# Kernel tuning notes

Hardware: AMD Instinct MI355X
Metric: run time of the kernel (lower is better)

Reference implementation:

```python
import jax, jax.numpy as jnp
import numpy as np

EPS = 1e-8
N, D, B, L = 50000, 128, 64, 512
P0, P1, NEG_MS = 200000, 50000, 4


def setup_inputs() -> dict:
    key = jax.random.key(0)
    ks = jax.random.split(key, 14)
    return {
        "embeddings": jax.random.normal(ks[0], (N, D), jnp.float32) * 0.1,
        "W_rep": jax.random.normal(ks[1], (D, 2), jnp.float32) * 0.01,
        "W_q": jax.random.normal(ks[2], (D, D), jnp.float32) * 0.01,
        "W_k": jax.random.normal(ks[3], (D, D), jnp.float32) * 0.01,
        "W_v": jax.random.normal(ks[4], (D, D), jnp.float32) * 0.01,
        "Head_agg": jax.random.normal(ks[5], (D, D), jnp.float32) * 0.01,
        "user_init": jax.random.normal(ks[6], (1, D), jnp.float32) * 0.01,
        "sd_e0": jnp.ones((), jnp.float32),
        "sd_e1": jnp.ones((), jnp.float32),
        "sd_seq": jnp.ones((), jnp.float32),
        "pos_e0": jax.random.randint(ks[7], (P0, 2), 0, N, jnp.int32),
        "neg_e0": jax.random.randint(ks[8], (P0, 2), 0, N, jnp.int32),
        "pos_e1": jax.random.randint(ks[9], (P1, 2), 0, N, jnp.int32),
        "neg_e1": jax.random.randint(ks[10], (P1 * NEG_MS, 2), 0, N, jnp.int32),
        "q_seqs": jax.random.randint(ks[11], (B, L), 0, N, jnp.int32),
        "c_seqs": jax.random.randint(ks[12], (B, L), 0, 2, jnp.int32),
        "neg_ms": NEG_MS,
    }


def _logsig(x):
    return jnp.log(jax.nn.sigmoid(x) + EPS)


def _task_term(loss, p_t, sd):
    return loss / (sd ** 2 + EPS) + p_t * jnp.log(sd + EPS)


def _forward(embeddings, W_rep, W_q, W_k, W_v, Head_agg, user_init,
             sd_e0, sd_e1, sd_seq,
             pos_e0, neg_e0, pos_e1, neg_e1, q_seqs, c_seqs, neg_ms):
    d = embeddings.shape[1]
    scale = 1.0 / jnp.sqrt(jnp.asarray(d, jnp.float32))

    # ---- edge type e0: complete ----
    ph0 = embeddings[pos_e0[:, 0]]
    pt0 = embeddings[pos_e0[:, 1]]
    nh0 = embeddings[neg_e0[:, 0]]
    nt0 = embeddings[neg_e0[:, 1]]
    pos_score0 = jnp.sum(ph0 * pt0, axis=1)
    neg_score0 = jnp.sum(nh0 * nt0, axis=1)
    loss0 = -(_logsig(pos_score0).sum() + _logsig(-neg_score0).sum())
    p_t0 = pos_e0.shape[0] + neg_e0.shape[0]
    tf_loss = _task_term(loss0, p_t0, sd_e0)

    # ---- edge type e1: incomplete (pairwise ranking) ----
    ph1 = jnp.tile(embeddings[pos_e1[:, 0]], (neg_ms, 1))   # [P1*neg_ms, D]
    pt1 = jnp.tile(embeddings[pos_e1[:, 1]], (neg_ms, 1))
    nh1 = embeddings[neg_e1[:, 0]]
    nt1 = embeddings[neg_e1[:, 1]]
    pos_score1 = jnp.sum(ph1 * pt1, axis=1)
    neg_score_h = jnp.sum(nh1 * pt1, axis=1)
    neg_score_t = jnp.sum(ph1 * nt1, axis=1)
    loss1 = -(_logsig(pos_score1 - neg_score_h).sum() +
              _logsig(pos_score1 - neg_score_t).sum())
    p_t1 = neg_e1.shape[0] * 2
    tf_loss = tf_loss + _task_term(loss1, p_t1, sd_e1)

    # ---- per-user single-head causal attention (batched via vmap) ----
    seq_len = q_seqs.shape[1]
    idx = jnp.arange(seq_len)
    # mask[i, j] = 0 if j >= i else -inf (softmax over i => attend to i <= j)
    mask = jnp.where(idx[:, None] <= idx[None, :], 0.0, -jnp.inf)

    def one_user(q_s, c_s):
        I_q = embeddings[q_s].T                 # [D, L]
        I = W_rep[:, c_s] + I_q                 # [D, L]
        q = W_q @ I                             # [D, L]
        k = W_k @ I
        v = W_v @ I
        score = (k.T @ q) * scale               # [L, L], score[i, j] = k_i . q_j
        att = jax.nn.softmax(score + mask, axis=0)
        b = v @ att                             # [D, L]
        o = Head_agg @ b                        # [D, L]
        u_state = jnp.concatenate([user_init, o.T], axis=0)  # [L+1, D]
        return u_state[:-1, :], I_q.T           # ([L, D], [L, D])

    u_state_b, q_state_b = jax.vmap(one_user)(q_seqs, c_seqs)  # [B, L, D]
    u_flat = u_state_b.reshape(-1, d)
    q_flat = q_state_b.reshape(-1, d)
    c_flat = c_seqs.reshape(-1).astype(jnp.float32)
    pred = jax.nn.sigmoid(jnp.sum(u_flat * q_flat, axis=1))
    seq_loss = -(c_flat * jnp.log(pred + EPS) +
                 (1.0 - c_flat) * jnp.log(1.0 - pred + EPS)).sum()
    p_t_seq = seq_len  # original uses length of the LAST user's sequence
    tf_loss = tf_loss + _task_term(seq_loss, p_t_seq, sd_seq)
    return tf_loss


def reference(embeddings, W_rep, W_q, W_k, W_v, Head_agg, user_init,
              sd_e0, sd_e1, sd_seq,
              pos_e0, neg_e0, pos_e1, neg_e1, q_seqs, c_seqs, neg_ms):
    return _forward(embeddings, W_rep, W_q, W_k, W_v, Head_agg, user_init,
                    sd_e0, sd_e1, sd_seq,
                    pos_e0, neg_e0, pos_e1, neg_e1, q_seqs, c_seqs, neg_ms)
```

## Files before the change

### kernel.cpp

```cpp
#include <hip/hip_runtime.h>
#include <hip/hip_bf16.h>

#define EPSF 1e-8f
#define NN 50000
#define DD 128
#define BB 64
#define LL 512
#define PP0 200000
#define PP1 50000
#define SCALE 0.08838834764831845f

typedef float f4v __attribute__((ext_vector_type(4)));
typedef short s8v __attribute__((ext_vector_type(8)));
typedef short s4v __attribute__((ext_vector_type(4)));

__device__ __forceinline__ float logsigf(float x) {
    float s = 1.f / (1.f + __expf(-x));
    return __logf(s + EPSF);
}

__device__ __forceinline__ float red64(float v) {
    #pragma unroll
    for (int m = 32; m >= 1; m >>= 1) v += __shfl_xor(v, m, 64);
    return v;
}
__device__ __forceinline__ float red16(float v) {
    #pragma unroll
    for (int m = 8; m >= 1; m >>= 1) v += __shfl_xor(v, m, 64);
    return v;
}
__device__ __forceinline__ float red8(float v) {
    #pragma unroll
    for (int m = 4; m >= 1; m >>= 1) v += __shfl_xor(v, m, 64);
    return v;
}

__device__ __forceinline__ void block_atomic_sum(float local, float* dst) {
    local = red64(local);
    __shared__ float w4[4];
    if ((threadIdx.x & 63) == 0) w4[threadIdx.x >> 6] = local;
    __syncthreads();
    if (threadIdx.x == 0) atomicAdd(dst, w4[0] + w4[1] + w4[2] + w4[3]);
}

__device__ __forceinline__ unsigned short f2bf(float f) {
    unsigned u = __float_as_uint(f);
    unsigned r = (u + 0x7fffu + ((u >> 16) & 1u)) >> 16;
    return (unsigned short)r;
}
__device__ __forceinline__ float bf2f(unsigned short u) {
    return __uint_as_float(((unsigned)u) << 16);
}

__device__ __forceinline__ float dot8bf(s8v a, s8v b) {
    float s = 0.f;
    #pragma unroll
    for (int j = 0; j < 8; j++)
        s += bf2f((unsigned short)a[j]) * bf2f((unsigned short)b[j]);
    return s;
}

__global__ __launch_bounds__(256) void cvt_emb_kernel(
    const float* __restrict__ emb, unsigned short* __restrict__ emb16)
{
    int stride = gridDim.x * 256 * 8;
    for (int i = (blockIdx.x * 256 + threadIdx.x) * 8; i < NN * DD; i += stride) {
        float4 a = *(const float4*)&emb[i];
        float4 b = *(const float4*)&emb[i + 4];
        s8v o;
        o[0] = (short)f2bf(a.x); o[1] = (short)f2bf(a.y);
        o[2] = (short)f2bf(a.z); o[3] = (short)f2bf(a.w);
        o[4] = (short)f2bf(b.x); o[5] = (short)f2bf(b.y);
        o[6] = (short)f2bf(b.z); o[7] = (short)f2bf(b.w);
        *(s8v*)&emb16[i] = o;
    }
}

__global__ __launch_bounds__(256) void cvt_w_kernel(
    const float* __restrict__ Wq, const float* __restrict__ Wk,
    const float* __restrict__ Wv, const float* __restrict__ Hd,
    unsigned short* __restrict__ W16)
{
    int idx = (blockIdx.x * 256 + threadIdx.x) * 8;
    int which = idx >> 14, off = idx & 16383;
    const float* src = (which == 0) ? Wq : (which == 1) ? Wk : (which == 2) ? Wv : Hd;
    float4 a = *(const float4*)&src[off];
    float4 b = *(const float4*)&src[off + 4];
    s8v o;
    o[0] = (short)f2bf(a.x); o[1] = (short)f2bf(a.y);
    o[2] = (short)f2bf(a.z); o[3] = (short)f2bf(a.w);
    o[4] = (short)f2bf(b.x); o[5] = (short)f2bf(b.y);
    o[6] = (short)f2bf(b.z); o[7] = (short)f2bf(b.w);
    *(s8v*)&W16[idx] = o;
}

#define E0B 1024
#define E1B 640
__global__ __launch_bounds__(256) void edges_kernel(
    const unsigned short* __restrict__ emb16, const int* __restrict__ pos,
    const int* __restrict__ neg, const int* __restrict__ pos1,
    const int* __restrict__ neg1, float* __restrict__ acc)
{
    if (blockIdx.x < E0B) {
        int sub = threadIdx.x & 7;
        int g0 = (blockIdx.x * 256 + threadIdx.x) >> 3;
        const int ng = E0B * 32;
        float local = 0.f;
        for (int grp = g0; grp < 2 * PP0; grp += ng) {
            bool isneg = grp >= PP0;
            const int* e = isneg ? (neg + 2 * (grp - PP0)) : (pos + 2 * grp);
            int h = e[0], t = e[1];
            const unsigned short* hr = emb16 + (size_t)h * DD + 16 * sub;
            const unsigned short* tr = emb16 + (size_t)t * DD + 16 * sub;
            s8v a0 = *(const s8v*)&hr[0];
            s8v a1 = *(const s8v*)&hr[8];
            s8v b0 = *(const s8v*)&tr[0];
            s8v b1 = *(const s8v*)&tr[8];
            float d = red8(dot8bf(a0, b0) + dot8bf(a1, b1));
            if (sub == 0) local += logsigf(isneg ? -d : d);
        }
        block_atomic_sum(local, acc);
    } else {
        int sub = threadIdx.x & 15;
        int g0 = ((blockIdx.x - E0B) * 256 + threadIdx.x) >> 4;
        const int ng = E1B * 16;
        float local = 0.f;
        for (int i = g0; i < PP1; i += ng) {
            int ph = pos1[2 * i], pt = pos1[2 * i + 1];
            s8v vph = *(const s8v*)&emb16[(size_t)ph * DD + 8 * sub];
            s8v vpt = *(const s8v*)&emb16[(size_t)pt * DD + 8 * sub];
            float ps = red16(dot8bf(vph, vpt));
            #pragma unroll
            for (int mloop = 0; mloop < 4; mloop++) {
                int g = mloop * PP1 + i;
                int nh = neg1[2 * g], nt = neg1[2 * g + 1];
                s8v vnh = *(const s8v*)&emb16[(size_t)nh * DD + 8 * sub];
                s8v vnt = *(const s8v*)&emb16[(size_t)nt * DD + 8 * sub];
                float sh = red16(dot8bf(vnh, vpt));
                float st = red16(dot8bf(vph, vnt));
                if (sub == 0) local += logsigf(ps - sh) + logsigf(ps - st);
            }
        }
        block_atomic_sum(local, acc + 1);
    }
}

__global__ __launch_bounds__(256) void proj_kernel(
    const unsigned short* __restrict__ emb16, const float* __restrict__ Wrep,
    const unsigned short* __restrict__ W16, const int* __restrict__ qseq,
    const int* __restrict__ cseq, unsigned short* __restrict__ QT16,
    unsigned short* __restrict__ KT16, unsigned short* __restrict__ VT16T)
{
    int b = blockIdx.y;
    int t0 = blockIdx.x * 64;
    __shared__ unsigned short Itok[64 * 136];
    __shared__ unsigned short Wl[128 * 136];
    __shared__ int qs[64];
    __shared__ int cs[64];
    int tid = threadIdx.x;
    if (tid < 64) {
        qs[tid] = qseq[b * LL + t0 + tid];
        cs[tid] = cseq[b * LL + t0 + tid];
    }
    __syncthreads();
    {
        int t = tid >> 2, d0 = (tid & 3) * 32;
        const unsigned short* er = emb16 + (size_t)qs[t] * DD + d0;
        int c = cs[t];
        #pragma unroll
        for (int e = 0; e < 32; e += 8) {
            s8v raw = *(const s8v*)&er[e];
            s8v o;
            #pragma unroll
            for (int j = 0; j < 8; j++) {
                float f = bf2f((unsigned short)raw[j]) + Wrep[(d0 + e + j) * 2 + c];
                o[j] = (short)f2bf(f);
            }
            *(s8v*)&Itok[t * 136 + d0 + e] = o;
        }
    }
    int w = tid >> 6, lane = tid & 63, n = lane & 15, quad = lane >> 4;

    for (int w3 = 0; w3 < 3; w3++) {
        __syncthreads();
        {
            const unsigned short* src = W16 + w3 * DD * DD + (tid >> 1) * DD + (tid & 1) * 64;
            unsigned short* dst = &Wl[(tid >> 1) * 136 + (tid & 1) * 64];
            #pragma unroll
            for (int e = 0; e < 64; e += 8)
                *(s8v*)&dst[e] = *(const s8v*)&src[e];
        }
        __syncthreads();
        f4v a2[2][4];
        #pragma unroll
        for (int mt = 0; mt < 2; mt++)
            #pragma unroll
            for (int nt = 0; nt < 4; nt++) a2[mt][nt] = (f4v){0.f, 0.f, 0.f, 0.f};
        #pragma unroll
        for (int c = 0; c < 4; c++) {
            s8v af0 = *(const s8v*)&Wl[(w * 32 + n) * 136 + c * 32 + quad * 8];
            s8v af1 = *(const s8v*)&Wl[(w * 32 + 16 + n) * 136 + c * 32 + quad * 8];
            #pragma unroll
            for (int nt = 0; nt < 4; nt++) {
                s8v bf = *(const s8v*)&Itok[(nt * 16 + n) * 136 + c * 32 + quad * 8];
                a2[0][nt] = __builtin_amdgcn_mfma_f32_16x16x32_bf16(af0, bf, a2[0][nt], 0, 0, 0);
                a2[1][nt] = __builtin_amdgcn_mfma_f32_16x16x32_bf16(af1, bf, a2[1][nt], 0, 0, 0);
            }
        }
        if (w3 < 2) {
            unsigned short* OUT = (w3 == 0) ? QT16 : KT16;
            #pragma unroll
            for (int mt = 0; mt < 2; mt++)
                #pragma unroll
                for (int nt = 0; nt < 4; nt++) {
                    int t = t0 + nt * 16 + n;
                    int r = w * 32 + mt * 16 + quad * 4;
                    s4v o;
                    #pragma unroll
                    for (int rr = 0; rr < 4; rr++) o[rr] = (short)f2bf(a2[mt][nt][rr]);
                    *(s4v*)&OUT[((size_t)(b * LL) + t) * DD + r] = o;
                }
        } else {
            __syncthreads();
            #pragma unroll
            for (int mt = 0; mt < 2; mt++)
                #pragma unroll
                for (int nt = 0; nt < 4; nt++) {
                    int tl = nt * 16 + n;
                    int r = w * 32 + mt * 16 + quad * 4;
                    #pragma unroll
                    for (int rr = 0; rr < 4; rr++)
                        Wl[(r + rr) * 72 + tl] = f2bf(a2[mt][nt][rr]);
                }
            __syncthreads();
            int row = tid >> 1, half = tid & 1;
            unsigned short* gdst = VT16T + ((size_t)b * DD + row) * LL + t0 + half * 32;
            const unsigned short* lsrc = &Wl[row * 72 + half * 32];
            #pragma unroll
            for (int e = 0; e < 32; e += 8)
                *(s8v*)&gdst[e] = *(const s8v*)&lsrc[e];
        }
    }
}

__global__ __launch_bounds__(256) void attn_mfma_kernel(
    const unsigned short* __restrict__ QT16, const unsigned short* __restrict__ KT16,
    const unsigned short* __restrict__ VT16T, float* __restrict__ BvT)
{
    int id = blockIdx.x;
    int r0 = id & 255;
    int b = r0 & 63;
    int qt = (id >> 8) ? (7 - (r0 >> 6)) : (r0 >> 6);

    __shared__ unsigned short K_lds[64 * 136];
    __shared__ unsigned short Vt_lds[128 * 72];
    __shared__ unsigned short P_lds[64 * 72];

    int tid = threadIdx.x;
    int w = tid >> 6;
    int lane = tid & 63;
    int n = lane & 15;
    int quad = lane >> 4;
    int gj = qt * 64 + w * 16 + n;

    s8v qfrag[4];
    {
        const unsigned short* qrow = QT16 + ((size_t)(b * LL) + gj) * DD;
        #pragma unroll
        for (int c = 0; c < 4; c++)
            qfrag[c] = *(const s8v*)&qrow[c * 32 + quad * 8];
    }

    f4v oacc[8];
    #pragma unroll
    for (int dt = 0; dt < 8; dt++) oacc[dt] = (f4v){0.f, 0.f, 0.f, 0.f};
    float m_run = -INFINITY, l_run = 0.f;

    s8v kreg[4], vreg[4];
    #pragma unroll
    for (int rep = 0; rep < 4; rep++) {
        int idx = rep * 2048 + tid * 8;
        int ki = idx >> 7, kd = idx & 127;
        kreg[rep] = *(const s8v*)&KT16[((size_t)(b * LL) + ki) * DD + kd];
        int vr = idx >> 6, vc = idx & 63;
        vreg[rep] = *(const s8v*)&VT16T[((size_t)b * DD + vr) * LL + vc];
    }

    for (int kt = 0; kt <= qt; ++kt) {
        __syncthreads();
        #pragma unroll
        for (int rep = 0; rep < 4; rep++) {
            int idx = rep * 2048 + tid * 8;
            int ki = idx >> 7, kd = idx & 127;
            *(s8v*)&K_lds[ki * 136 + kd] = kreg[rep];
            int vr = idx >> 6, vc = idx & 63;
            *(s8v*)&Vt_lds[vr * 72 + vc] = vreg[rep];
        }
        __syncthreads();
        if (kt < qt) {
            #pragma unroll
            for (int rep = 0; rep < 4; rep++) {
                int idx = rep * 2048 + tid * 8;
                int ki = idx >> 7, kd = idx & 127;
                kreg[rep] = *(const s8v*)&KT16[((size_t)(b * LL) + (kt + 1) * 64 + ki) * DD + kd];
                int vr = idx >> 6, vc = idx & 63;
                vreg[rep] = *(const s8v*)&VT16T[((size_t)b * DD + vr) * LL + (kt + 1) * 64 + vc];
            }
        }

        f4v sacc[4];
        #pragma unroll
        for (int mt = 0; mt < 4; mt++) sacc[mt] = (f4v){0.f, 0.f, 0.f, 0.f};
        #pragma unroll
        for (int c = 0; c < 4; c++) {
            #pragma unroll
            for (int mt = 0; mt < 4; mt++) {
                s8v af = *(const s8v*)&K_lds[(mt * 16 + n) * 136 + c * 32 + quad * 8];
                sacc[mt] = __builtin_amdgcn_mfma_f32_16x16x32_bf16(af, qfrag[c], sacc[mt], 0, 0, 0);
            }
        }

        bool diag = (kt == qt);
        float mloc = -INFINITY;
        #pragma unroll
        for (int mt = 0; mt < 4; mt++) {
            #pragma unroll
            for (int rr = 0; rr < 4; rr++) {
                float s = sacc[mt][rr] * SCALE;
                if (diag && (kt * 64 + mt * 16 + quad * 4 + rr) > gj) s = -INFINITY;
                sacc[mt][rr] = s;
                mloc = fmaxf(mloc, s);
            }
        }
        mloc = fmaxf(mloc, __shfl_xor(mloc, 16));
        mloc = fmaxf(mloc, __shfl_xor(mloc, 32));
        float mnew = fmaxf(m_run, mloc);
        float alpha = __expf(m_run - mnew);
        m_run = mnew;

        float rsum = 0.f;
        #pragma unroll
        for (int mt = 0; mt < 4; mt++) {
            s4v pp;
            #pragma unroll
            for (int rr = 0; rr < 4; rr++) {
                float p = __expf(sacc[mt][rr] - mnew);
                rsum += p;
                pp[rr] = (short)f2bf(p);
            }
            *(s4v*)&P_lds[(w * 16 + n) * 72 + mt * 16 + quad * 4] = pp;
        }
        rsum += __shfl_xor(rsum, 16);
        rsum += __shfl_xor(rsum, 32);
        l_run = l_run * alpha + rsum;

        #pragma unroll
        for (int rr = 0; rr < 4; rr++) {
            float a_r = __shfl(alpha, quad * 4 + rr);
            #pragma unroll
            for (int dt = 0; dt < 8; dt++) oacc[dt][rr] *= a_r;
        }

        #pragma unroll
        for (int cc = 0; cc < 2; cc++) {
            s8v pf = *(const s8v*)&P_lds[(w * 16 + n) * 72 + cc * 32 + quad * 8];
            #pragma unroll
            for (int dt = 0; dt < 8; dt++) {
                s8v vf = *(const s8v*)&Vt_lds[(dt * 16 + n) * 72 + cc * 32 + quad * 8];
                oacc[dt] = __builtin_amdgcn_mfma_f32_16x16x32_bf16(pf, vf, oacc[dt], 0, 0, 0);
            }
        }
    }

    float linv = 1.f / l_run;
    #pragma unroll
    for (int rr = 0; rr < 4; rr++) {
        float li = __shfl(linv, quad * 4 + rr);
        int t = qt * 64 + w * 16 + quad * 4 + rr;
        float* orow = BvT + ((size_t)(b * LL) + t) * DD;
        #pragma unroll
        for (int dt = 0; dt < 8; dt++)
            orow[dt * 16 + n] = oacc[dt][rr] * li;
    }
}

__global__ __launch_bounds__(256) void head_kernel(
    const unsigned short* __restrict__ H16, const float* __restrict__ BvT,
    const unsigned short* __restrict__ emb16, const float* __restrict__ uinit,
    const int* __restrict__ qseq, const int* __restrict__ cseq,
    float* __restrict__ acc)
{
    int b = blockIdx.y;
    int t0 = blockIdx.x * 64;
    __shared__ unsigned short Btok[64 * 136];
    __shared__ unsigned short Hl[128 * 136];
    __shared__ unsigned short O_lds[64 * 136];
    int tid = threadIdx.x;
    {
        int t = tid >> 2, d0 = (tid & 3) * 32;
        const float* br = BvT + ((size_t)(b * LL) + t0 + t) * DD + d0;
        #pragma unroll
        for (int e = 0; e < 32; e += 8) {
            float4 x = *(const float4*)&br[e];
            float4 y = *(const float4*)&br[e + 4];
            s8v o;
            o[0] = (short)f2bf(x.x); o[1] = (short)f2bf(x.y);
            o[2] = (short)f2bf(x.z); o[3] = (short)f2bf(x.w);
            o[4] = (short)f2bf(y.x); o[5] = (short)f2bf(y.y);
            o[6] = (short)f2bf(y.z); o[7] = (short)f2bf(y.w);
            *(s8v*)&Btok[t * 136 + d0 + e] = o;
        }
    }
    {
        const unsigned short* src = H16 + (tid >> 1) * DD + (tid & 1) * 64;
        unsigned short* dst = &Hl[(tid >> 1) * 136 + (tid & 1) * 64];
        #pragma unroll
        for (int e = 0; e < 64; e += 8)
            *(s8v*)&dst[e] = *(const s8v*)&src[e];
    }
    __syncthreads();

    int w = tid >> 6, lane = tid & 63, n = lane & 15, quad = lane >> 4;
    f4v a2[2][4];
    #pragma unroll
    for (int mt = 0; mt < 2; mt++)
        #pragma unroll
        for (int nt = 0; nt < 4; nt++) a2[mt][nt] = (f4v){0.f, 0.f, 0.f, 0.f};
    #pragma unroll
    for (int c = 0; c < 4; c++) {
        s8v af0 = *(const s8v*)&Hl[(w * 32 + n) * 136 + c * 32 + quad * 8];
        s8v af1 = *(const s8v*)&Hl[(w * 32 + 16 + n) * 136 + c * 32 + quad * 8];
        #pragma unroll
        for (int nt = 0; nt < 4; nt++) {
            s8v bf = *(const s8v*)&Btok[(nt * 16 + n) * 136 + c * 32 + quad * 8];
            a2[0][nt] = __builtin_amdgcn_mfma_f32_16x16x32_bf16(af0, bf, a2[0][nt], 0, 0, 0);
            a2[1][nt] = __builtin_amdgcn_mfma_f32_16x16x32_bf16(af1, bf, a2[1][nt], 0, 0, 0);
        }
    }
    #pragma unroll
    for (int mt = 0; mt < 2; mt++)
        #pragma unroll
        for (int nt = 0; nt < 4; nt++) {
            int tl = nt * 16 + n;
            int r = w * 32 + mt * 16 + quad * 4;
            #pragma unroll
            for (int rr = 0; rr < 4; rr++)
                O_lds[tl * 136 + r + rr] = f2bf(a2[mt][nt][rr]);
        }
    __syncthreads();

    int g = tid >> 4, sub = tid & 15;
    float local = 0.f;
    #pragma unroll
    for (int tt = 0; tt < 4; tt++) {
        int tl = g * 4 + tt;
        int t = t0 + tl + 1;
        if (t < LL) {
            s8v uv = *(const s8v*)&O_lds[tl * 136 + sub * 8];
            int qi = qseq[b * LL + t];
            s8v ev = *(const s8v*)&emb16[(size_t)qi * DD + sub * 8];
            float s = red16(dot8bf(uv, ev));
            if (sub == 0) {
                float c = (float)cseq[b * LL + t];
                float pred = 1.f / (1.f + __expf(-s));
                local += c * __logf(pred + EPSF) + (1.f - c) * __logf(1.f - pred + EPSF);
            }
        }
    }
    if (t0 == 0 && g == 0) {
        int qi = qseq[b * LL];
        s8v ev = *(const s8v*)&emb16[(size_t)qi * DD + sub * 8];
        float4 u0 = *(const float4*)&uinit[sub * 8];
        float4 u1 = *(const float4*)&uinit[sub * 8 + 4];
        float s = u0.x * bf2f((unsigned short)ev[0]) + u0.y * bf2f((unsigned short)ev[1])
                + u0.z * bf2f((unsigned short)ev[2]) + u0.w * bf2f((unsigned short)ev[3])
                + u1.x * bf2f((unsigned short)ev[4]) + u1.y * bf2f((unsigned short)ev[5])
                + u1.z * bf2f((unsigned short)ev[6]) + u1.w * bf2f((unsigned short)ev[7]);
        s = red16(s);
        if (sub == 0) {
            float c = (float)cseq[b * LL];
            float pred = 1.f / (1.f + __expf(-s));
            local += c * __logf(pred + EPSF) + (1.f - c) * __logf(1.f - pred + EPSF);
        }
    }
    block_atomic_sum(local, acc + 2);
}

__global__ void combine_kernel(
    const float* __restrict__ acc, const float* __restrict__ sd0p,
    const float* __restrict__ sd1p, const float* __restrict__ sdqp,
    float* __restrict__ out)
{
    if (threadIdx.x == 0 && blockIdx.x == 0) {
        float l0 = -acc[0], l1 = -acc[1], ls = -acc[2];
        float s0 = *sd0p, s1 = *sd1p, ss = *sdqp;
        float tf = l0 / (s0 * s0 + EPSF) + 400000.f * logf(s0 + EPSF)
                 + l1 / (s1 * s1 + EPSF) + 400000.f * logf(s1 + EPSF)
                 + ls / (ss * ss + EPSF) + 512.f * logf(ss + EPSF);
        out[0] = tf;
    }
}

extern "C" void kernel_launch(void* const* d_in, const int* in_sizes, int n_in,
                              void* d_out, int out_size, void* d_ws, size_t ws_size,
                              hipStream_t stream) {
    const float* emb   = (const float*)d_in[0];
    const float* Wrep  = (const float*)d_in[1];
    const float* Wq    = (const float*)d_in[2];
    const float* Wk    = (const float*)d_in[3];
    const float* Wv    = (const float*)d_in[4];
    const float* Hd    = (const float*)d_in[5];
    const float* uinit = (const float*)d_in[6];
    const float* sd0   = (const float*)d_in[7];
    const float* sd1   = (const float*)d_in[8];
    const float* sdq   = (const float*)d_in[9];
    const int* pe0 = (const int*)d_in[10];
    const int* ne0 = (const int*)d_in[11];
    const int* pe1 = (const int*)d_in[12];
    const int* ne1 = (const int*)d_in[13];
    const int* qs  = (const int*)d_in[14];
    const int* cs  = (const int*)d_in[15];

    const size_t SZ = (size_t)BB * LL * DD;
    char* base = (char*)d_ws;
    float* acc = (float*)base;
    unsigned short* emb16 = (unsigned short*)(base + 256);
    unsigned short* W16   = emb16 + (size_t)NN * DD;
    unsigned short* QT16  = W16 + 4 * DD * DD;
    unsigned short* KT16  = QT16 + SZ;
    unsigned short* VT16T = KT16 + SZ;
    float* BvT = (float*)(VT16T + SZ);

    hipMemsetAsync(acc, 0, 256, stream);

    cvt_emb_kernel<<<1024, 256, 0, stream>>>(emb, emb16);
    cvt_w_kernel<<<32, 256, 0, stream>>>(Wq, Wk, Wv, Hd, W16);

    edges_kernel<<<E0B + E1B, 256, 0, stream>>>(emb16, pe0, ne0, pe1, ne1, acc);

    proj_kernel<<<dim3(8, 64), 256, 0, stream>>>(emb16, Wrep, W16, qs, cs,
                                                 QT16, KT16, VT16T);
    attn_mfma_kernel<<<512, 256, 0, stream>>>(QT16, KT16, VT16T, BvT);
    head_kernel<<<dim3(8, 64), 256, 0, stream>>>(W16 + 3 * DD * DD, BvT,
                                                 emb16, uinit, qs, cs, acc);

    combine_kernel<<<1, 64, 0, stream>>>(acc, sd0, sd1, sdq, (float*)d_out);
}
```

Before: 206.4 us.

## Spread edge-loss blocks across projection, attention and head kernels

Removes the standalone edges kernel and splits its 1664 blocks among the proj, attn and head launches as extra blocks (416+896+352), so the irregular gather-bound edge work runs alongside the compute-bound sequence kernels. Also removes the weight conversion kernel by converting fp32 weights to bf16 while staging them into LDS, and reuses Btok in place of a separate O_lds buffer. This saves launches and fills idle CUs, but adds redundant weight conversion per block and risks load imbalance or lower occupancy in the fused kernels.

```diff
diff --git a/kernel.cpp b/kernel.cpp
--- a/kernel.cpp
+++ b/kernel.cpp
@@ -10,6 +10,12 @@
 #define PP1 50000
 #define SCALE 0.08838834764831845f
 
+#define G0B 1024
+#define G1B 640
+#define EK2 416
+#define EK3 896
+#define EK4 352
+
 typedef float f4v __attribute__((ext_vector_type(4)));
 typedef short s8v __attribute__((ext_vector_type(8)));
 typedef short s4v __attribute__((ext_vector_type(4)));
@@ -58,6 +64,55 @@
     for (int j = 0; j < 8; j++)
         s += bf2f((unsigned short)a[j]) * bf2f((unsigned short)b[j]);
     return s;
+}
+
+__device__ void edge_slice(int eid, const unsigned short* __restrict__ emb16,
+                           const int* __restrict__ pos, const int* __restrict__ neg,
+                           const int* __restrict__ pos1, const int* __restrict__ neg1,
+                           float* __restrict__ acc)
+{
+    if (eid < G0B) {
+        int sub = threadIdx.x & 7;
+        int g0 = eid * 32 + (threadIdx.x >> 3);
+        const int ng = G0B * 32;
+        float local = 0.f;
+        for (int grp = g0; grp < 2 * PP0; grp += ng) {
+            bool isneg = grp >= PP0;
+            const int* e = isneg ? (neg + 2 * (grp - PP0)) : (pos + 2 * grp);
+            int h = e[0], t = e[1];
+            const unsigned short* hr = emb16 + (size_t)h * DD + 16 * sub;
+            const unsigned short* tr = emb16 + (size_t)t * DD + 16 * sub;
+            s8v a0 = *(const s8v*)&hr[0];
+            s8v a1 = *(const s8v*)&hr[8];
+            s8v b0 = *(const s8v*)&tr[0];
+            s8v b1 = *(const s8v*)&tr[8];
+            float d = red8(dot8bf(a0, b0) + dot8bf(a1, b1));
+            if (sub == 0) local += logsigf(isneg ? -d : d);
+        }
+        block_atomic_sum(local, acc);
+    } else {
+        int sub = threadIdx.x & 15;
+        int g0 = (eid - G0B) * 16 + (threadIdx.x >> 4);
+        const int ng = G1B * 16;
+        float local = 0.f;
+        for (int i = g0; i < PP1; i += ng) {
+            int ph = pos1[2 * i], pt = pos1[2 * i + 1];
+            s8v vph = *(const s8v*)&emb16[(size_t)ph * DD + 8 * sub];
+            s8v vpt = *(const s8v*)&emb16[(size_t)pt * DD + 8 * sub];
+            float ps = red16(dot8bf(vph, vpt));
+            #pragma unroll
+            for (int mloop = 0; mloop < 4; mloop++) {
+                int g = mloop * PP1 + i;
+                int nh = neg1[2 * g], nt = neg1[2 * g + 1];
+                s8v vnh = *(const s8v*)&emb16[(size_t)nh * DD + 8 * sub];
+                s8v vnt = *(const s8v*)&emb16[(size_t)nt * DD + 8 * sub];
+                float sh = red16(dot8bf(vnh, vpt));
+                float st = red16(dot8bf(vph, vnt));
+                if (sub == 0) local += logsigf(ps - sh) + logsigf(ps - st);
+            }
+        }
+        block_atomic_sum(local, acc + 1);
+    }
 }
 
 __global__ __launch_bounds__(256) void cvt_emb_kernel(
@@ -76,83 +131,22 @@
     }
 }
 
-__global__ __launch_bounds__(256) void cvt_w_kernel(
+__global__ __launch_bounds__(256) void proj_edges_kernel(
+    const unsigned short* __restrict__ emb16, const float* __restrict__ Wrep,
     const float* __restrict__ Wq, const float* __restrict__ Wk,
-    const float* __restrict__ Wv, const float* __restrict__ Hd,
-    unsigned short* __restrict__ W16)
+    const float* __restrict__ Wv, const int* __restrict__ qseq,
+    const int* __restrict__ cseq, unsigned short* __restrict__ QT16,
+    unsigned short* __restrict__ KT16, unsigned short* __restrict__ VT16T,
+    const int* __restrict__ pos, const int* __restrict__ neg,
+    const int* __restrict__ pos1, const int* __restrict__ neg1,
+    float* __restrict__ acc)
 {
-    int idx = (blockIdx.x * 256 + threadIdx.x) * 8;
-    int which = idx >> 14, off = idx & 16383;
-    const float* src = (which == 0) ? Wq : (which == 1) ? Wk : (which == 2) ? Wv : Hd;
-    float4 a = *(const float4*)&src[off];
-    float4 b = *(const float4*)&src[off + 4];
-    s8v o;
-    o[0] = (short)f2bf(a.x); o[1] = (short)f2bf(a.y);
-    o[2] = (short)f2bf(a.z); o[3] = (short)f2bf(a.w);
-    o[4] = (short)f2bf(b.x); o[5] = (short)f2bf(b.y);
-    o[6] = (short)f2bf(b.z); o[7] = (short)f2bf(b.w);
-    *(s8v*)&W16[idx] = o;
-}
-
-#define E0B 1024
-#define E1B 640
-__global__ __launch_bounds__(256) void edges_kernel(
-    const unsigned short* __restrict__ emb16, const int* __restrict__ pos,
-    const int* __restrict__ neg, const int* __restrict__ pos1,
-    const int* __restrict__ neg1, float* __restrict__ acc)
-{
-    if (blockIdx.x < E0B) {
-        int sub = threadIdx.x & 7;
-        int g0 = (blockIdx.x * 256 + threadIdx.x) >> 3;
-        const int ng = E0B * 32;
-        float local = 0.f;
-        for (int grp = g0; grp < 2 * PP0; grp += ng) {
-            bool isneg = grp >= PP0;
-            const int* e = isneg ? (neg + 2 * (grp - PP0)) : (pos + 2 * grp);
-            int h = e[0], t = e[1];
-            const unsigned short* hr = emb16 + (size_t)h * DD + 16 * sub;
-            const unsigned short* tr = emb16 + (size_t)t * DD + 16 * sub;
-            s8v a0 = *(const s8v*)&hr[0];
-            s8v a1 = *(const s8v*)&hr[8];
-            s8v b0 = *(const s8v*)&tr[0];
-            s8v b1 = *(const s8v*)&tr[8];
-            float d = red8(dot8bf(a0, b0) + dot8bf(a1, b1));
-            if (sub == 0) local += logsigf(isneg ? -d : d);
-        }
-        block_atomic_sum(local, acc);
-    } else {
-        int sub = threadIdx.x & 15;
-        int g0 = ((blockIdx.x - E0B) * 256 + threadIdx.x) >> 4;
-        const int ng = E1B * 16;
-        float local = 0.f;
-        for (int i = g0; i < PP1; i += ng) {
-            int ph = pos1[2 * i], pt = pos1[2 * i + 1];
-            s8v vph = *(const s8v*)&emb16[(size_t)ph * DD + 8 * sub];
-            s8v vpt = *(const s8v*)&emb16[(size_t)pt * DD + 8 * sub];
-            float ps = red16(dot8bf(vph, vpt));
-            #pragma unroll
-            for (int mloop = 0; mloop < 4; mloop++) {
-                int g = mloop * PP1 + i;
-                int nh = neg1[2 * g], nt = neg1[2 * g + 1];
-                s8v vnh = *(const s8v*)&emb16[(size_t)nh * DD + 8 * sub];
-                s8v vnt = *(const s8v*)&emb16[(size_t)nt * DD + 8 * sub];
-                float sh = red16(dot8bf(vnh, vpt));
-                float st = red16(dot8bf(vph, vnt));
-                if (sub == 0) local += logsigf(ps - sh) + logsigf(ps - st);
-            }
-        }
-        block_atomic_sum(local, acc + 1);
-    }
-}
-
-__global__ __launch_bounds__(256) void proj_kernel(
-    const unsigned short* __restrict__ emb16, const float* __restrict__ Wrep,
-    const unsigned short* __restrict__ W16, const int* __restrict__ qseq,
-    const int* __restrict__ cseq, unsigned short* __restrict__ QT16,
-    unsigned short* __restrict__ KT16, unsigned short* __restrict__ VT16T)
-{
-    int b = blockIdx.y;
-    int t0 = blockIdx.x * 64;
+    if (blockIdx.x >= 512) {
+        edge_slice(blockIdx.x - 512, emb16, pos, neg, pos1, neg1, acc);
+        return;
+    }
+    int b = blockIdx.x >> 3;
+    int t0 = (blockIdx.x & 7) << 6;
     __shared__ unsigned short Itok[64 * 136];
     __shared__ unsigned short Wl[128 * 136];
     __shared__ int qs[64];
@@ -182,13 +176,22 @@
     int w = tid >> 6, lane = tid & 63, n = lane & 15, quad = lane >> 4;
 
     for (int w3 = 0; w3 < 3; w3++) {
+        const float* Wsel = (w3 == 0) ? Wq : (w3 == 1) ? Wk : Wv;
         __syncthreads();
         {
-            const unsigned short* src = W16 + w3 * DD * DD + (tid >> 1) * DD + (tid & 1) * 64;
+            const float* src = Wsel + (tid >> 1) * DD + (tid & 1) * 64;
             unsigned short* dst = &Wl[(tid >> 1) * 136 + (tid & 1) * 64];
             #pragma unroll
-            for (int e = 0; e < 64; e += 8)
-                *(s8v*)&dst[e] = *(const s8v*)&src[e];
+            for (int e = 0; e < 64; e += 8) {
+                float4 x = *(const float4*)&src[e];
+                float4 y = *(const float4*)&src[e + 4];
+                s8v o;
+                o[0] = (short)f2bf(x.x); o[1] = (short)f2bf(x.y);
+                o[2] = (short)f2bf(x.z); o[3] = (short)f2bf(x.w);
+                o[4] = (short)f2bf(y.x); o[5] = (short)f2bf(y.y);
+                o[6] = (short)f2bf(y.z); o[7] = (short)f2bf(y.w);
+                *(s8v*)&dst[e] = o;
+            }
         }
         __syncthreads();
         f4v a2[2][4];
@@ -243,10 +246,18 @@
     }
 }
 
-__global__ __launch_bounds__(256) void attn_mfma_kernel(
+__global__ __launch_bounds__(256) void attn_edges_kernel(
     const unsigned short* __restrict__ QT16, const unsigned short* __restrict__ KT16,
-    const unsigned short* __restrict__ VT16T, float* __restrict__ BvT)
+    const unsigned short* __restrict__ VT16T, float* __restrict__ BvT,
+    const unsigned short* __restrict__ emb16,
+    const int* __restrict__ pos, const int* __restrict__ neg,
+    const int* __restrict__ pos1, const int* __restrict__ neg1,
+    float* __restrict__ acc)
 {
+    if (blockIdx.x >= 512) {
+        edge_slice(EK2 + (blockIdx.x - 512), emb16, pos, neg, pos1, neg1, acc);
+        return;
+    }
     int id = blockIdx.x;
     int r0 = id & 255;
     int b = r0 & 63;
@@ -384,17 +395,22 @@
     }
 }
 
-__global__ __launch_bounds__(256) void head_kernel(
-    const unsigned short* __restrict__ H16, const float* __restrict__ BvT,
+__global__ __launch_bounds__(256) void head_edges_kernel(
+    const float* __restrict__ Hd, const float* __restrict__ BvT,
     const unsigned short* __restrict__ emb16, const float* __restrict__ uinit,
     const int* __restrict__ qseq, const int* __restrict__ cseq,
+    const int* __restrict__ pos, const int* __restrict__ neg,
+    const int* __restrict__ pos1, const int* __restrict__ neg1,
     float* __restrict__ acc)
 {
-    int b = blockIdx.y;
-    int t0 = blockIdx.x * 64;
+    if (blockIdx.x >= 512) {
+        edge_slice(EK2 + EK3 + (blockIdx.x - 512), emb16, pos, neg, pos1, neg1, acc);
+        return;
+    }
+    int b = blockIdx.x >> 3;
+    int t0 = (blockIdx.x & 7) << 6;
     __shared__ unsigned short Btok[64 * 136];
     __shared__ unsigned short Hl[128 * 136];
-    __shared__ unsigned short O_lds[64 * 136];
     int tid = threadIdx.x;
     {
         int t = tid >> 2, d0 = (tid & 3) * 32;
@@ -412,11 +428,19 @@
         }
     }
     {
-        const unsigned short* src = H16 + (tid >> 1) * DD + (tid & 1) * 64;
+        const float* src = Hd + (tid >> 1) * DD + (tid & 1) * 64;
         unsigned short* dst = &Hl[(tid >> 1) * 136 + (tid & 1) * 64];
         #pragma unroll
-        for (int e = 0; e < 64; e += 8)
-            *(s8v*)&dst[e] = *(const s8v*)&src[e];
+        for (int e = 0; e < 64; e += 8) {
+            float4 x = *(const float4*)&src[e];
+            float4 y = *(const float4*)&src[e + 4];
+            s8v o;
+            o[0] = (short)f2bf(x.x); o[1] = (short)f2bf(x.y);
+            o[2] = (short)f2bf(x.z); o[3] = (short)f2bf(x.w);
+            o[4] = (short)f2bf(y.x); o[5] = (short)f2bf(y.y);
+            o[6] = (short)f2bf(y.z); o[7] = (short)f2bf(y.w);
+            *(s8v*)&dst[e] = o;
+        }
     }
     __syncthreads();
 
@@ -437,6 +461,7 @@
             a2[1][nt] = __builtin_amdgcn_mfma_f32_16x16x32_bf16(af1, bf, a2[1][nt], 0, 0, 0);
         }
     }
+    __syncthreads();
     #pragma unroll
     for (int mt = 0; mt < 2; mt++)
         #pragma unroll
@@ -445,7 +470,7 @@
             int r = w * 32 + mt * 16 + quad * 4;
             #pragma unroll
             for (int rr = 0; rr < 4; rr++)
-                O_lds[tl * 136 + r + rr] = f2bf(a2[mt][nt][rr]);
+                Btok[tl * 136 + r + rr] = f2bf(a2[mt][nt][rr]);
         }
     __syncthreads();
 
@@ -456,7 +481,7 @@
         int tl = g * 4 + tt;
         int t = t0 + tl + 1;
         if (t < LL) {
-            s8v uv = *(const s8v*)&O_lds[tl * 136 + sub * 8];
+            s8v uv = *(const s8v*)&Btok[tl * 136 + sub * 8];
             int qi = qseq[b * LL + t];
             s8v ev = *(const s8v*)&emb16[(size_t)qi * DD + sub * 8];
             float s = red16(dot8bf(uv, ev));
@@ -525,8 +550,7 @@
     char* base = (char*)d_ws;
     float* acc = (float*)base;
     unsigned short* emb16 = (unsigned short*)(base + 256);
-    unsigned short* W16   = emb16 + (size_t)NN * DD;
-    unsigned short* QT16  = W16 + 4 * DD * DD;
+    unsigned short* QT16  = emb16 + (size_t)NN * DD;
     unsigned short* KT16  = QT16 + SZ;
     unsigned short* VT16T = KT16 + SZ;
     float* BvT = (float*)(VT16T + SZ);
@@ -534,15 +558,14 @@
     hipMemsetAsync(acc, 0, 256, stream);
 
     cvt_emb_kernel<<<1024, 256, 0, stream>>>(emb, emb16);
-    cvt_w_kernel<<<32, 256, 0, stream>>>(Wq, Wk, Wv, Hd, W16);
-
-    edges_kernel<<<E0B + E1B, 256, 0, stream>>>(emb16, pe0, ne0, pe1, ne1, acc);
-
-    proj_kernel<<<dim3(8, 64), 256, 0, stream>>>(emb16, Wrep, W16, qs, cs,
-                                                 QT16, KT16, VT16T);
-    attn_mfma_kernel<<<512, 256, 0, stream>>>(QT16, KT16, VT16T, BvT);
-    head_kernel<<<dim3(8, 64), 256, 0, stream>>>(W16 + 3 * DD * DD, BvT,
-                                                 emb16, uinit, qs, cs, acc);
+
+    proj_edges_kernel<<<512 + EK2, 256, 0, stream>>>(
+        emb16, Wrep, Wq, Wk, Wv, qs, cs, QT16, KT16, VT16T,
+        pe0, ne0, pe1, ne1, acc);
+    attn_edges_kernel<<<512 + EK3, 256, 0, stream>>>(
+        QT16, KT16, VT16T, BvT, emb16, pe0, ne0, pe1, ne1, acc);
+    head_edges_kernel<<<512 + EK4, 256, 0, stream>>>(
+        Hd, BvT, emb16, uinit, qs, cs, pe0, ne0, pe1, ne1, acc);
 
     combine_kernel<<<1, 64, 0, stream>>>(acc, sd0, sd1, sdq, (float*)d_out);
 }
```

New measurement: 224.7 us. 8.9% more time.

## Fuse head projection into attention kernel and drop weight conversion kernel

Applied to the files above, without the earlier changes.

Merges the attention kernel and the head/loss kernel. Each attention block now writes its normalized output as bf16 into shared memory, applies Head_agg there in two 64-row passes, and computes the sequence loss in place, so the fp32 BvT round trip through global memory and one launch go away. The separate weight-conversion kernel is also removed. Weights are now converted from fp32 to bf16 inline while being staged into shared memory in proj and the fused kernel. The cost is more shared-memory aliasing in one larger kernel, and each block redoes the Head_agg conversion.

```diff
diff --git a/kernel.cpp b/kernel.cpp
--- a/kernel.cpp
+++ b/kernel.cpp
@@ -9,6 +9,9 @@
 #define PP0 200000
 #define PP1 50000
 #define SCALE 0.08838834764831845f
+
+#define E0B 1024
+#define E1B 640
 
 typedef float f4v __attribute__((ext_vector_type(4)));
 typedef short s8v __attribute__((ext_vector_type(8)));
@@ -76,26 +79,6 @@
     }
 }
 
-__global__ __launch_bounds__(256) void cvt_w_kernel(
-    const float* __restrict__ Wq, const float* __restrict__ Wk,
-    const float* __restrict__ Wv, const float* __restrict__ Hd,
-    unsigned short* __restrict__ W16)
-{
-    int idx = (blockIdx.x * 256 + threadIdx.x) * 8;
-    int which = idx >> 14, off = idx & 16383;
-    const float* src = (which == 0) ? Wq : (which == 1) ? Wk : (which == 2) ? Wv : Hd;
-    float4 a = *(const float4*)&src[off];
-    float4 b = *(const float4*)&src[off + 4];
-    s8v o;
-    o[0] = (short)f2bf(a.x); o[1] = (short)f2bf(a.y);
-    o[2] = (short)f2bf(a.z); o[3] = (short)f2bf(a.w);
-    o[4] = (short)f2bf(b.x); o[5] = (short)f2bf(b.y);
-    o[6] = (short)f2bf(b.z); o[7] = (short)f2bf(b.w);
-    *(s8v*)&W16[idx] = o;
-}
-
-#define E0B 1024
-#define E1B 640
 __global__ __launch_bounds__(256) void edges_kernel(
     const unsigned short* __restrict__ emb16, const int* __restrict__ pos,
     const int* __restrict__ neg, const int* __restrict__ pos1,
@@ -147,7 +130,8 @@
 
 __global__ __launch_bounds__(256) void proj_kernel(
     const unsigned short* __restrict__ emb16, const float* __restrict__ Wrep,
-    const unsigned short* __restrict__ W16, const int* __restrict__ qseq,
+    const float* __restrict__ Wq, const float* __restrict__ Wk,
+    const float* __restrict__ Wv, const int* __restrict__ qseq,
     const int* __restrict__ cseq, unsigned short* __restrict__ QT16,
     unsigned short* __restrict__ KT16, unsigned short* __restrict__ VT16T)
 {
@@ -182,13 +166,22 @@
     int w = tid >> 6, lane = tid & 63, n = lane & 15, quad = lane >> 4;
 
     for (int w3 = 0; w3 < 3; w3++) {
+        const float* Wsel = (w3 == 0) ? Wq : (w3 == 1) ? Wk : Wv;
         __syncthreads();
         {
-            const unsigned short* src = W16 + w3 * DD * DD + (tid >> 1) * DD + (tid & 1) * 64;
+            const float* src = Wsel + (tid >> 1) * DD + (tid & 1) * 64;
             unsigned short* dst = &Wl[(tid >> 1) * 136 + (tid & 1) * 64];
             #pragma unroll
-            for (int e = 0; e < 64; e += 8)
-                *(s8v*)&dst[e] = *(const s8v*)&src[e];
+            for (int e = 0; e < 64; e += 8) {
+                float4 x = *(const float4*)&src[e];
+                float4 y = *(const float4*)&src[e + 4];
+                s8v o;
+                o[0] = (short)f2bf(x.x); o[1] = (short)f2bf(x.y);
+                o[2] = (short)f2bf(x.z); o[3] = (short)f2bf(x.w);
+                o[4] = (short)f2bf(y.x); o[5] = (short)f2bf(y.y);
+                o[6] = (short)f2bf(y.z); o[7] = (short)f2bf(y.w);
+                *(s8v*)&dst[e] = o;
+            }
         }
         __syncthreads();
         f4v a2[2][4];
@@ -243,18 +236,25 @@
     }
 }
 
-__global__ __launch_bounds__(256) void attn_mfma_kernel(
+__global__ __launch_bounds__(256) void attn_head_kernel(
     const unsigned short* __restrict__ QT16, const unsigned short* __restrict__ KT16,
-    const unsigned short* __restrict__ VT16T, float* __restrict__ BvT)
+    const unsigned short* __restrict__ VT16T, const float* __restrict__ Hd,
+    const unsigned short* __restrict__ emb16, const float* __restrict__ uinit,
+    const int* __restrict__ qseq, const int* __restrict__ cseq,
+    float* __restrict__ acc)
 {
+    __shared__ unsigned short U[26112];
+    unsigned short* K_lds  = U;
+    unsigned short* Vt_lds = U + 8704;
+    unsigned short* P_lds  = U + 17920;
+    unsigned short* Bv_lds = U;
+    unsigned short* Hl     = U + 8704;
+    unsigned short* O_lds  = U + 17408;
+
     int id = blockIdx.x;
     int r0 = id & 255;
     int b = r0 & 63;
     int qt = (id >> 8) ? (7 - (r0 >> 6)) : (r0 >> 6);
-
-    __shared__ unsigned short K_lds[64 * 136];
-    __shared__ unsigned short Vt_lds[128 * 72];
-    __shared__ unsigned short P_lds[64 * 72];
 
     int tid = threadIdx.x;
     int w = tid >> 6;
@@ -372,89 +372,67 @@
         }
     }
 
-    float linv = 1.f / l_run;
-    #pragma unroll
-    for (int rr = 0; rr < 4; rr++) {
-        float li = __shfl(linv, quad * 4 + rr);
-        int t = qt * 64 + w * 16 + quad * 4 + rr;
-        float* orow = BvT + ((size_t)(b * LL) + t) * DD;
-        #pragma unroll
-        for (int dt = 0; dt < 8; dt++)
-            orow[dt * 16 + n] = oacc[dt][rr] * li;
-    }
-}
-
-__global__ __launch_bounds__(256) void head_kernel(
-    const unsigned short* __restrict__ H16, const float* __restrict__ BvT,
-    const unsigned short* __restrict__ emb16, const float* __restrict__ uinit,
-    const int* __restrict__ qseq, const int* __restrict__ cseq,
-    float* __restrict__ acc)
-{
-    int b = blockIdx.y;
-    int t0 = blockIdx.x * 64;
-    __shared__ unsigned short Btok[64 * 136];
-    __shared__ unsigned short Hl[128 * 136];
-    __shared__ unsigned short O_lds[64 * 136];
-    int tid = threadIdx.x;
+    __syncthreads();
     {
-        int t = tid >> 2, d0 = (tid & 3) * 32;
-        const float* br = BvT + ((size_t)(b * LL) + t0 + t) * DD + d0;
-        #pragma unroll
-        for (int e = 0; e < 32; e += 8) {
-            float4 x = *(const float4*)&br[e];
-            float4 y = *(const float4*)&br[e + 4];
-            s8v o;
-            o[0] = (short)f2bf(x.x); o[1] = (short)f2bf(x.y);
-            o[2] = (short)f2bf(x.z); o[3] = (short)f2bf(x.w);
-            o[4] = (short)f2bf(y.x); o[5] = (short)f2bf(y.y);
-            o[6] = (short)f2bf(y.z); o[7] = (short)f2bf(y.w);
-            *(s8v*)&Btok[t * 136 + d0 + e] = o;
-        }
-    }
-    {
-        const unsigned short* src = H16 + (tid >> 1) * DD + (tid & 1) * 64;
-        unsigned short* dst = &Hl[(tid >> 1) * 136 + (tid & 1) * 64];
-        #pragma unroll
-        for (int e = 0; e < 64; e += 8)
-            *(s8v*)&dst[e] = *(const s8v*)&src[e];
-    }
-    __syncthreads();
-
-    int w = tid >> 6, lane = tid & 63, n = lane & 15, quad = lane >> 4;
-    f4v a2[2][4];
-    #pragma unroll
-    for (int mt = 0; mt < 2; mt++)
-        #pragma unroll
-        for (int nt = 0; nt < 4; nt++) a2[mt][nt] = (f4v){0.f, 0.f, 0.f, 0.f};
-    #pragma unroll
-    for (int c = 0; c < 4; c++) {
-        s8v af0 = *(const s8v*)&Hl[(w * 32 + n) * 136 + c * 32 + quad * 8];
-        s8v af1 = *(const s8v*)&Hl[(w * 32 + 16 + n) * 136 + c * 32 + quad * 8];
-        #pragma unroll
-        for (int nt = 0; nt < 4; nt++) {
-            s8v bf = *(const s8v*)&Btok[(nt * 16 + n) * 136 + c * 32 + quad * 8];
-            a2[0][nt] = __builtin_amdgcn_mfma_f32_16x16x32_bf16(af0, bf, a2[0][nt], 0, 0, 0);
-            a2[1][nt] = __builtin_amdgcn_mfma_f32_16x16x32_bf16(af1, bf, a2[1][nt], 0, 0, 0);
-        }
-    }
-    #pragma unroll
-    for (int mt = 0; mt < 2; mt++)
+        float linv = 1.f / l_run;
+        #pragma unroll
+        for (int rr = 0; rr < 4; rr++) {
+            float li = __shfl(linv, quad * 4 + rr);
+            int tl = w * 16 + quad * 4 + rr;
+            #pragma unroll
+            for (int dt = 0; dt < 8; dt++)
+                Bv_lds[tl * 136 + dt * 16 + n] = f2bf(oacc[dt][rr] * li);
+        }
+    }
+
+    #pragma unroll
+    for (int pass = 0; pass < 2; pass++) {
+        __syncthreads();
+        {
+            int r = tid >> 2, d0 = (tid & 3) * 32;
+            const float* src = Hd + (size_t)(pass * 64 + r) * DD + d0;
+            #pragma unroll
+            for (int e = 0; e < 32; e += 8) {
+                float4 x = *(const float4*)&src[e];
+                float4 y = *(const float4*)&src[e + 4];
+                s8v o;
+                o[0] = (short)f2bf(x.x); o[1] = (short)f2bf(x.y);
+                o[2] = (short)f2bf(x.z); o[3] = (short)f2bf(x.w);
+                o[4] = (short)f2bf(y.x); o[5] = (short)f2bf(y.y);
+                o[6] = (short)f2bf(y.z); o[7] = (short)f2bf(y.w);
+                *(s8v*)&Hl[r * 136 + d0 + e] = o;
+            }
+        }
+        __syncthreads();
+        f4v o2[4];
+        #pragma unroll
+        for (int nt = 0; nt < 4; nt++) o2[nt] = (f4v){0.f, 0.f, 0.f, 0.f};
+        #pragma unroll
+        for (int c = 0; c < 4; c++) {
+            s8v af = *(const s8v*)&Hl[(w * 16 + n) * 136 + c * 32 + quad * 8];
+            #pragma unroll
+            for (int nt = 0; nt < 4; nt++) {
+                s8v bf = *(const s8v*)&Bv_lds[(nt * 16 + n) * 136 + c * 32 + quad * 8];
+                o2[nt] = __builtin_amdgcn_mfma_f32_16x16x32_bf16(af, bf, o2[nt], 0, 0, 0);
+            }
+        }
+        int rbase = pass * 64 + w * 16 + quad * 4;
         #pragma unroll
         for (int nt = 0; nt < 4; nt++) {
             int tl = nt * 16 + n;
-            int r = w * 32 + mt * 16 + quad * 4;
             #pragma unroll
             for (int rr = 0; rr < 4; rr++)
-                O_lds[tl * 136 + r + rr] = f2bf(a2[mt][nt][rr]);
-        }
+                O_lds[tl * 136 + rbase + rr] = f2bf(o2[nt][rr]);
+        }
+    }
     __syncthreads();
 
-    int g = tid >> 4, sub = tid & 15;
+    int g2 = tid >> 4, sub = tid & 15;
     float local = 0.f;
     #pragma unroll
     for (int tt = 0; tt < 4; tt++) {
-        int tl = g * 4 + tt;
-        int t = t0 + tl + 1;
+        int tl = g2 * 4 + tt;
+        int t = qt * 64 + tl + 1;
         if (t < LL) {
             s8v uv = *(const s8v*)&O_lds[tl * 136 + sub * 8];
             int qi = qseq[b * LL + t];
@@ -467,7 +445,7 @@
             }
         }
     }
-    if (t0 == 0 && g == 0) {
+    if (qt == 0 && g2 == 0) {
         int qi = qseq[b * LL];
         s8v ev = *(const s8v*)&emb16[(size_t)qi * DD + sub * 8];
         float4 u0 = *(const float4*)&uinit[sub * 8];
@@ -525,24 +503,20 @@
     char* base = (char*)d_ws;
     float* acc = (float*)base;
     unsigned short* emb16 = (unsigned short*)(base + 256);
-    unsigned short* W16   = emb16 + (size_t)NN * DD;
-    unsigned short* QT16  = W16 + 4 * DD * DD;
+    unsigned short* QT16  = emb16 + (size_t)NN * DD;
     unsigned short* KT16  = QT16 + SZ;
     unsigned short* VT16T = KT16 + SZ;
-    float* BvT = (float*)(VT16T + SZ);
 
     hipMemsetAsync(acc, 0, 256, stream);
 
     cvt_emb_kernel<<<1024, 256, 0, stream>>>(emb, emb16);
-    cvt_w_kernel<<<32, 256, 0, stream>>>(Wq, Wk, Wv, Hd, W16);
 
     edges_kernel<<<E0B + E1B, 256, 0, stream>>>(emb16, pe0, ne0, pe1, ne1, acc);
 
-    proj_kernel<<<dim3(8, 64), 256, 0, stream>>>(emb16, Wrep, W16, qs, cs,
-                                                 QT16, KT16, VT16T);
-    attn_mfma_kernel<<<512, 256, 0, stream>>>(QT16, KT16, VT16T, BvT);
-    head_kernel<<<dim3(8, 64), 256, 0, stream>>>(W16 + 3 * DD * DD, BvT,
-                                                 emb16, uinit, qs, cs, acc);
+    proj_kernel<<<dim3(8, 64), 256, 0, stream>>>(emb16, Wrep, Wq, Wk, Wv,
+                                                 qs, cs, QT16, KT16, VT16T);
+    attn_head_kernel<<<512, 256, 0, stream>>>(QT16, KT16, VT16T, Hd, emb16,
+                                              uinit, qs, cs, acc);
 
     combine_kernel<<<1, 64, 0, stream>>>(acc, sd0, sd1, sdq, (float*)d_out);
 }
```

Result: no change. 203.1 us (-1.6%).
